# Performance work log

Hardware: AMD Instinct MI355X
Metric: run time of the kernel (lower is better)

Reference implementation:

```python
import jax, jax.numpy as jnp
import numpy as np

N = 500_000
D = 256
G = 1024


def setup_inputs() -> dict:
    key = jax.random.key(0)
    k1, k2, k3, k4, k5, k6 = jax.random.split(key, 6)
    x = jax.random.normal(k1, (N, D), dtype=jnp.float32)
    batch = jnp.sort(jax.random.randint(k2, (N,), 0, G).astype(jnp.int64))
    s = 1.0 / np.sqrt(D)
    W1 = jax.random.normal(k3, (D, D), dtype=jnp.float32) * s
    b1 = jax.random.normal(k4, (D,), dtype=jnp.float32) * 0.01
    W2 = jax.random.normal(k5, (D, 1), dtype=jnp.float32) * s
    b2 = jax.random.normal(k6, (1,), dtype=jnp.float32) * 0.01
    return {"x": x, "batch": batch, "num_graphs": G,
            "W1": W1, "b1": b1, "W2": W2, "b2": b2}


def reference(x, batch, num_graphs, W1, b1, W2, b2):
    # gate MLP: Linear -> Tanh -> Linear  => [N, 1]
    h = jnp.tanh(x @ W1 + b1)
    scores = (h @ W2 + b2)[:, 0]  # [N]
    # segment softmax over nodes grouped by graph id
    seg_max = jax.ops.segment_max(scores, batch, num_segments=num_graphs)  # [G]
    # empty segments give -inf max, but no node indexes them
    e = jnp.exp(scores - seg_max[batch])  # [N]
    denom = jax.ops.segment_sum(e, batch, num_segments=num_graphs)  # [G]
    attn = e / denom[batch]  # [N]
    weighted = x * attn[:, None]  # [N, D]
    # global_add_pool: scatter-add nodes into graphs
    return jax.ops.segment_sum(weighted, batch, num_segments=num_graphs)  # [G, D]
```

## Files before the change

### kernel.cpp

```cpp
#include <hip/hip_runtime.h>

#define D 256
#define ROWS 32
#define NBLK 512

typedef __attribute__((ext_vector_type(8))) short bf16x8;
typedef __attribute__((ext_vector_type(4))) float f32x4;

__device__ __forceinline__ unsigned short f2bf(float a) {
    unsigned int u = __float_as_uint(a);
    u = (u + 0x7fffu + ((u >> 16) & 1u)) >> 16;
    return (unsigned short)u;
}

__device__ __forceinline__ unsigned int cvt_pk_bf16(float a, float b) {
    unsigned int r;
    asm("v_cvt_pk_bf16_f32 %0, %1, %2" : "=v"(r) : "v"(a), "v"(b));
    return r;
}

__device__ __forceinline__ float fast_tanh(float v) {
    float a = __builtin_fabsf(v);
    float e = __builtin_amdgcn_exp2f(a * -2.88539008177793f);
    float t = (1.0f - e) * __builtin_amdgcn_rcpf(1.0f + e);
    return __builtin_copysignf(t, v);
}

__device__ __forceinline__ int xf_off(int c, int r, int q) {
    return ((c << 10) + (r << 5) + (q << 4)) ^ ((c & 3) << 5) ^ ((r & 4) << 2);
}

__device__ __forceinline__ void gload_lds16(const void* g, void* l) {
    __builtin_amdgcn_global_load_lds(
        (const __attribute__((address_space(1))) unsigned int*)g,
        (__attribute__((address_space(3))) unsigned int*)l, 16, 0, 0);
}

__global__ void pack_w1_k(const float* __restrict__ W1, unsigned short* __restrict__ W1p) {
    int p = blockIdx.x * 256 + threadIdx.x;
    int e  = p & 7;
    int l  = (p >> 3) & 63;
    int cb = (p >> 9) & 15;
    int kk = p >> 13;
    int k   = 32 * kk + 8 * (l >> 4) + e;
    int col = 16 * cb + (l & 15);
    W1p[p] = f2bf(W1[k * D + col]);
}

__global__ void zero_k(float* __restrict__ p, int n) {
    int i = blockIdx.x * 256 + threadIdx.x;
    if (i < n) p[i] = 0.f;
}

#define STAGE(XN, tn) do {                                                      \
    const int _r0s = (tn) * ROWS;                                               \
    _Pragma("unroll")                                                           \
    for (int _it = 0; _it < 8; ++_it) {                                         \
        const int _c = _it * 4 + w;                                             \
        const int _r = (l >> 1) ^ (_c & 3);                                     \
        const int _q = (l & 1) ^ ((_r >> 2) & 1);                               \
        int _row = _r0s + _r; _row = (_row < N) ? _row : (N - 1);               \
        gload_lds16((const char*)x + ((size_t)_row << 10) + (size_t)(((_c << 1) + _q) << 4), \
                    (char*)(XN) + (_it << 12) + (w << 10) + (l << 4));          \
    }                                                                           \
} while (0)

#define FLUSHX() do {                                                           \
    *reinterpret_cast<float4*>(&red[w][l * 4]) = a4;                            \
    int _m8 = 0x7fffffff;                                                       \
    _Pragma("unroll")                                                           \
    for (int _it = 0; _it < 8; ++_it)                                           \
        if (bg[_it] > g_cur && bg[_it] < _m8) _m8 = bg[_it];                    \
    _m8 = min(_m8, __shfl_xor(_m8, 1));  _m8 = min(_m8, __shfl_xor(_m8, 2));    \
    _m8 = min(_m8, __shfl_xor(_m8, 4));  _m8 = min(_m8, __shfl_xor(_m8, 8));    \
    _m8 = min(_m8, __shfl_xor(_m8, 16)); _m8 = min(_m8, __shfl_xor(_m8, 32));   \
    float _dw = den_p;                                                          \
    _dw += __shfl_xor(_dw, 1);  _dw += __shfl_xor(_dw, 2);                      \
    _dw += __shfl_xor(_dw, 4);  _dw += __shfl_xor(_dw, 8);                      \
    _dw += __shfl_xor(_dw, 16); _dw += __shfl_xor(_dw, 32);                     \
    if (l == 0) { gmin4[w] = _m8; denw[w] = _dw; }                              \
    asm volatile("s_waitcnt lgkmcnt(0)" ::: "memory");                          \
    __builtin_amdgcn_sched_barrier(0);                                          \
    __builtin_amdgcn_s_barrier();                                               \
    __builtin_amdgcn_sched_barrier(0);                                          \
    { const float _fs = red[0][tid] + red[1][tid] + red[2][tid] + red[3][tid];  \
      atomicAdd(&accb[(size_t)g_cur * D + tid], _fs); }                         \
    if (tid == 0)                                                               \
        atomicAdd(&den[g_cur], (denw[0] + denw[1] + denw[2] + denw[3]) * 0.015625f); \
    gnv = min(min(gmin4[0], gmin4[1]), min(gmin4[2], gmin4[3]));                \
    a4 = make_float4(0.f, 0.f, 0.f, 0.f); den_p = 0.f;                          \
    __builtin_amdgcn_s_barrier();                                               \
    __builtin_amdgcn_sched_barrier(0);                                          \
} while (0)

#define POOL(XC) do {                                                           \
    if (g_cur < 0) g_cur = g0u;                                                 \
    while (true) {                                                              \
        _Pragma("unroll")                                                       \
        for (int _it = 0; _it < 8; ++_it) {                                     \
            const int _r = 4 * _it + w;                                         \
            const float _e = (bg[_it] == g_cur) ? erow[_r] : 0.f;               \
            const float4 _v = *reinterpret_cast<const float4*>(                 \
                (const char*)(XC) + xf_off(l >> 1, _r, l & 1));                 \
            a4.x += _e * _v.x; a4.y += _e * _v.y;                               \
            a4.z += _e * _v.z; a4.w += _e * _v.w;                               \
            den_p += _e;                                                        \
        }                                                                       \
        if (glast <= g_cur) break;                                              \
        FLUSHX();                                                               \
        g_cur = gnv;                                                            \
    }                                                                           \
} while (0)

#define BODY(XC, XN) do {                                                       \
    const int _row0 = t * ROWS;                                                 \
    _Pragma("unroll")                                                           \
    for (int _it = 0; _it < 8; ++_it) {                                         \
        int _ri = _row0 + 4 * _it + w;                                          \
        bg[_it] = batch[_ri < N ? _ri : N - 1];                                 \
    }                                                                           \
    const int g0u = batch[_row0];                                               \
    int _gli = _row0 + 31;                                                      \
    const int glast = batch[_gli < N ? _gli : N - 1];                           \
    __builtin_amdgcn_sched_barrier(0);                                          \
    const bool _hn = (t + 1 < t1);                                              \
    if (_hn) {                                                                  \
        STAGE(XN, t + 1);                                                       \
        asm volatile("s_waitcnt vmcnt(8) lgkmcnt(0)" ::: "memory");             \
    } else {                                                                    \
        asm volatile("s_waitcnt vmcnt(0) lgkmcnt(0)" ::: "memory");             \
    }                                                                           \
    __builtin_amdgcn_sched_barrier(0);                                          \
    __builtin_amdgcn_s_barrier();                                               \
    __builtin_amdgcn_sched_barrier(0);                                          \
     \
    f32x4 acc[2][4];                                                            \
    _Pragma("unroll")                                                           \
    for (int _m = 0; _m < 2; ++_m)                                              \
        _Pragma("unroll")                                                       \
        for (int _n = 0; _n < 4; ++_n) acc[_m][_n] = (f32x4){0.f, 0.f, 0.f, 0.f}; \
    _Pragma("unroll")                                                           \
    for (int _kk = 0; _kk < 8; ++_kk) {                                         \
        bf16x8 _afr[2];                                                         \
        _Pragma("unroll")                                                       \
        for (int _m = 0; _m < 2; ++_m) {                                        \
            const int _rr = 16 * _m + l15;                                      \
            const int _cc = 4 * _kk + g4;                                       \
            const int _o0 = xf_off(_cc, _rr, 0);                                \
            const float4 _f0 = *reinterpret_cast<const float4*>((const char*)(XC) + _o0); \
            const float4 _f1 = *reinterpret_cast<const float4*>((const char*)(XC) + (_o0 ^ 16)); \
            uint4 _u;                                                           \
            _u.x = cvt_pk_bf16(_f0.x, _f0.y); _u.y = cvt_pk_bf16(_f0.z, _f0.w); \
            _u.z = cvt_pk_bf16(_f1.x, _f1.y); _u.w = cvt_pk_bf16(_f1.z, _f1.w); \
            _afr[_m] = *reinterpret_cast<bf16x8*>(&_u);                         \
        }                                                                       \
        _Pragma("unroll")                                                       \
        for (int _m = 0; _m < 2; ++_m)                                          \
            _Pragma("unroll")                                                   \
            for (int _n = 0; _n < 4; ++_n)                                      \
                acc[_m][_n] = __builtin_amdgcn_mfma_f32_16x16x32_bf16(          \
                    _afr[_m], bfr[_kk * 4 + _n], acc[_m][_n], 0, 0, 0);         \
    }                                                                           \
    {                                                                           \
        float _part[2][4];                                                      \
        _Pragma("unroll")                                                       \
        for (int _m = 0; _m < 2; ++_m)                                          \
            _Pragma("unroll")                                                   \
            for (int _r = 0; _r < 4; ++_r) _part[_m][_r] = 0.f;                 \
        _Pragma("unroll")                                                       \
        for (int _n = 0; _n < 4; ++_n)                                          \
            _Pragma("unroll")                                                   \
            for (int _m = 0; _m < 2; ++_m)                                      \
                _Pragma("unroll")                                               \
                for (int _r = 0; _r < 4; ++_r) {                                \
                    float _h = fast_tanh(acc[_m][_n][_r] + b1v[_n]);            \
                    _part[_m][_r] += _h * w2v[_n];                              \
                }                                                               \
        _Pragma("unroll")                                                       \
        for (int _m = 0; _m < 2; ++_m)                                          \
            _Pragma("unroll")                                                   \
            for (int _r = 0; _r < 4; ++_r) {                                    \
                float _p = _part[_m][_r];                                       \
                _p += __shfl_xor(_p, 8, 16); _p += __shfl_xor(_p, 4, 16);       \
                _p += __shfl_xor(_p, 2, 16); _p += __shfl_xor(_p, 1, 16);       \
                if (l15 == 0) scpart[w][16 * _m + 4 * g4 + _r] = _p;            \
            }                                                                   \
    }                                                                           \
    asm volatile("s_waitcnt lgkmcnt(0)" ::: "memory");                          \
    __builtin_amdgcn_sched_barrier(0);                                          \
    __builtin_amdgcn_s_barrier();                                               \
    __builtin_amdgcn_sched_barrier(0);                                          \
    if (tid < 32) {                                                             \
        float _s = scpart[0][tid] + scpart[1][tid] + scpart[2][tid] + scpart[3][tid] + b2v; \
        erow[tid] = ((_row0 + tid) < N)                                         \
                  ? __builtin_amdgcn_exp2f(_s * 1.4426950408889634f) : 0.f;     \
    }                                                                           \
    asm volatile("s_waitcnt lgkmcnt(0)" ::: "memory");                          \
    __builtin_amdgcn_sched_barrier(0);                                          \
    __builtin_amdgcn_s_barrier();                                               \
    __builtin_amdgcn_sched_barrier(0);                                          \
    POOL(XC);                                                                   \
    asm volatile("s_waitcnt lgkmcnt(0)" ::: "memory");                          \
    __builtin_amdgcn_sched_barrier(0);                                          \
    __builtin_amdgcn_s_barrier();                                               \
    __builtin_amdgcn_sched_barrier(0);                                          \
    ++t;                                                                        \
} while (0)

__global__ void __launch_bounds__(256, 2)
fused_k(const float* __restrict__ x,
        const unsigned short* __restrict__ W1p,
        const float* __restrict__ b1,
        const float* __restrict__ W2,
        const float* __restrict__ b2,
        const int* __restrict__ batch,
        int N, int NT,
        float* __restrict__ accb, float* __restrict__ den) {
    __shared__ __align__(16) char Xf0[32768];
    __shared__ __align__(16) char Xf1[32768];
    __shared__ __align__(16) float red[4][256];
    __shared__ float scpart[4][32];
    __shared__ float erow[32];
    __shared__ int   gmin4[4];
    __shared__ float denw[4];

    const int tid = threadIdx.x;
    const int w   = tid >> 6;
    const int l   = tid & 63;
    const int l15 = l & 15;
    const int g4  = l >> 4;

    const int tpb = (NT + NBLK - 1) / NBLK;
    int t = blockIdx.x * tpb;
    const int t1 = min(NT, t + tpb);
    if (t >= t1) return;

    bf16x8 bfr[32];
    #pragma unroll
    for (int kk = 0; kk < 8; ++kk)
        #pragma unroll
        for (int n = 0; n < 4; ++n)
            bfr[kk * 4 + n] = *reinterpret_cast<const bf16x8*>(
                W1p + (size_t)(((kk * 16) + (w * 4 + n)) * 64 + l) * 8);

    float b1v[4], w2v[4];
    #pragma unroll
    for (int n = 0; n < 4; ++n) {
        int col = 64 * w + 16 * n + l15;
        b1v[n] = b1[col];
        w2v[n] = W2[col];
    }
    const float b2v = b2[0];

    STAGE(Xf0, t);

    float4 a4 = make_float4(0.f, 0.f, 0.f, 0.f);
    float den_p = 0.f;
    int g_cur = -1;
    int gnv = 0;
    int bg[8];

    while (true) {
        BODY(Xf0, Xf1);
        if (t >= t1) break;
        BODY(Xf1, Xf0);
        if (t >= t1) break;
    }

    FLUSHX();
}

__global__ void __launch_bounds__(256)
norm_k(const float* __restrict__ accb, const float* __restrict__ den,
       float* __restrict__ out) {
    int g = blockIdx.x;
    float dv = den[g];
    float inv = (dv > 0.f) ? 1.0f / dv : 0.f;
    out[(size_t)g * D + threadIdx.x] = accb[(size_t)g * D + threadIdx.x] * inv;
}

extern "C" void kernel_launch(void* const* d_in, const int* in_sizes, int n_in,
                              void* d_out, int out_size, void* d_ws, size_t ws_size,
                              hipStream_t stream) {
    const float* x     = (const float*)d_in[0];
    const int*   batch = (const int*)d_in[1];
    const float* W1    = (const float*)d_in[3];
    const float* b1    = (const float*)d_in[4];
    const float* W2    = (const float*)d_in[5];
    const float* b2    = (const float*)d_in[6];
    float* out = (float*)d_out;

    const int N = in_sizes[0] / D;
    const int G = out_size / D;
    const int NT = (N + ROWS - 1) / ROWS;

    char* ws = (char*)d_ws;
    unsigned short* W1p = (unsigned short*)ws;
    float* accb = (float*)(ws + 131072);
    float* den  = (float*)(ws + 131072 + (size_t)G * D * 4);

    zero_k<<<dim3((G * D + G + 255) / 256), dim3(256), 0, stream>>>(accb, G * D + G);
    pack_w1_k<<<dim3(256), dim3(256), 0, stream>>>(W1, W1p);
    fused_k<<<dim3(min(NBLK, NT)), dim3(256), 0, stream>>>(x, W1p, b1, W2, b2, batch,
                                                           N, NT, accb, den);
    norm_k<<<dim3(G), dim3(256), 0, stream>>>(accb, den, out);
}
```

Baseline: 189.2 us.

## Stage x through registers as bf16 LDS tiles, stream W1 from global, raise occupancy

```diff
diff --git a/kernel.cpp b/kernel.cpp
--- a/kernel.cpp
+++ b/kernel.cpp
@@ -2,7 +2,7 @@
 
 #define D 256
 #define ROWS 32
-#define NBLK 512
+#define NBLK 768
 
 typedef __attribute__((ext_vector_type(8))) short bf16x8;
 typedef __attribute__((ext_vector_type(4))) float f32x4;
@@ -26,14 +26,8 @@
     return __builtin_copysignf(t, v);
 }
 
-__device__ __forceinline__ int xf_off(int c, int r, int q) {
-    return ((c << 10) + (r << 5) + (q << 4)) ^ ((c & 3) << 5) ^ ((r & 4) << 2);
-}
-
-__device__ __forceinline__ void gload_lds16(const void* g, void* l) {
-    __builtin_amdgcn_global_load_lds(
-        (const __attribute__((address_space(1))) unsigned int*)g,
-        (__attribute__((address_space(3))) unsigned int*)l, 16, 0, 0);
+__device__ __forceinline__ int xb_off(int r, int kc) {
+    return (r << 9) + ((kc << 4) ^ ((r & 7) << 4));
 }
 
 __global__ void pack_w1_k(const float* __restrict__ W1, unsigned short* __restrict__ W1p) {
@@ -52,16 +46,24 @@
     if (i < n) p[i] = 0.f;
 }
 
-#define STAGE(XN, tn) do {                                                      \
+#define STAGELOAD(XV, tn) do {                                                  \
     const int _r0s = (tn) * ROWS;                                               \
     _Pragma("unroll")                                                           \
     for (int _it = 0; _it < 8; ++_it) {                                         \
-        const int _c = _it * 4 + w;                                             \
-        const int _r = (l >> 1) ^ (_c & 3);                                     \
-        const int _q = (l & 1) ^ ((_r >> 2) & 1);                               \
-        int _row = _r0s + _r; _row = (_row < N) ? _row : (N - 1);               \
-        gload_lds16((const char*)x + ((size_t)_row << 10) + (size_t)(((_c << 1) + _q) << 4), \
-                    (char*)(XN) + (_it << 12) + (w << 10) + (l << 4));          \
+        int _row = _r0s + 4 * _it + w;                                          \
+        _row = (_row < N) ? _row : (N - 1);                                     \
+        XV[_it] = x4[(size_t)_row * 64 + l];                                    \
+    }                                                                           \
+} while (0)
+
+#define WRITELDS(LN, XV) do {                                                   \
+    _Pragma("unroll")                                                           \
+    for (int _it = 0; _it < 8; ++_it) {                                         \
+        const int _r = 4 * _it + w;                                             \
+        uint2 _u = make_uint2(cvt_pk_bf16(XV[_it].x, XV[_it].y),                \
+                              cvt_pk_bf16(XV[_it].z, XV[_it].w));               \
+        *reinterpret_cast<uint2*>((char*)(LN) +                                 \
+            ((_r << 9) + ((l << 3) ^ ((_r & 7) << 4)))) = _u;                   \
     }                                                                           \
 } while (0)
 
@@ -79,31 +81,24 @@
     _dw += __shfl_xor(_dw, 4);  _dw += __shfl_xor(_dw, 8);                      \
     _dw += __shfl_xor(_dw, 16); _dw += __shfl_xor(_dw, 32);                     \
     if (l == 0) { gmin4[w] = _m8; denw[w] = _dw; }                              \
-    asm volatile("s_waitcnt lgkmcnt(0)" ::: "memory");                          \
-    __builtin_amdgcn_sched_barrier(0);                                          \
-    __builtin_amdgcn_s_barrier();                                               \
-    __builtin_amdgcn_sched_barrier(0);                                          \
+    __syncthreads();                                                            \
     { const float _fs = red[0][tid] + red[1][tid] + red[2][tid] + red[3][tid];  \
       atomicAdd(&accb[(size_t)g_cur * D + tid], _fs); }                         \
     if (tid == 0)                                                               \
         atomicAdd(&den[g_cur], (denw[0] + denw[1] + denw[2] + denw[3]) * 0.015625f); \
     gnv = min(min(gmin4[0], gmin4[1]), min(gmin4[2], gmin4[3]));                \
     a4 = make_float4(0.f, 0.f, 0.f, 0.f); den_p = 0.f;                          \
-    __builtin_amdgcn_s_barrier();                                               \
-    __builtin_amdgcn_sched_barrier(0);                                          \
-} while (0)
-
-#define POOL(XC) do {                                                           \
+    __syncthreads();                                                            \
+} while (0)
+
+#define POOL(XV) do {                                                           \
     if (g_cur < 0) g_cur = g0u;                                                 \
     while (true) {                                                              \
         _Pragma("unroll")                                                       \
         for (int _it = 0; _it < 8; ++_it) {                                     \
-            const int _r = 4 * _it + w;                                         \
-            const float _e = (bg[_it] == g_cur) ? erow[_r] : 0.f;               \
-            const float4 _v = *reinterpret_cast<const float4*>(                 \
-                (const char*)(XC) + xf_off(l >> 1, _r, l & 1));                 \
-            a4.x += _e * _v.x; a4.y += _e * _v.y;                               \
-            a4.z += _e * _v.z; a4.w += _e * _v.w;                               \
+            const float _e = (bg[_it] == g_cur) ? erow[4 * _it + w] : 0.f;      \
+            a4.x += _e * XV[_it].x; a4.y += _e * XV[_it].y;                     \
+            a4.z += _e * XV[_it].z; a4.w += _e * XV[_it].w;                     \
             den_p += _e;                                                        \
         }                                                                       \
         if (glast <= g_cur) break;                                              \
@@ -112,7 +107,7 @@
     }                                                                           \
 } while (0)
 
-#define BODY(XC, XN) do {                                                       \
+#define BODY(LC, LN, XVC, XVN) do {                                             \
     const int _row0 = t * ROWS;                                                 \
     _Pragma("unroll")                                                           \
     for (int _it = 0; _it < 8; ++_it) {                                         \
@@ -120,47 +115,45 @@
         bg[_it] = batch[_ri < N ? _ri : N - 1];                                 \
     }                                                                           \
     const int g0u = batch[_row0];                                               \
-    int _gli = _row0 + 31;                                                      \
+    int _gli = _row0 + ROWS - 1;                                                \
     const int glast = batch[_gli < N ? _gli : N - 1];                           \
-    __builtin_amdgcn_sched_barrier(0);                                          \
     const bool _hn = (t + 1 < t1);                                              \
-    if (_hn) {                                                                  \
-        STAGE(XN, t + 1);                                                       \
-        asm volatile("s_waitcnt vmcnt(8) lgkmcnt(0)" ::: "memory");             \
-    } else {                                                                    \
-        asm volatile("s_waitcnt vmcnt(0) lgkmcnt(0)" ::: "memory");             \
-    }                                                                           \
-    __builtin_amdgcn_sched_barrier(0);                                          \
-    __builtin_amdgcn_s_barrier();                                               \
-    __builtin_amdgcn_sched_barrier(0);                                          \
+    __syncthreads();       \
      \
     f32x4 acc[2][4];                                                            \
     _Pragma("unroll")                                                           \
     for (int _m = 0; _m < 2; ++_m)                                              \
         _Pragma("unroll")                                                       \
         for (int _n = 0; _n < 4; ++_n) acc[_m][_n] = (f32x4){0.f, 0.f, 0.f, 0.f}; \
+    bf16x8 _bc[4], _bn[4];                                                      \
+    _Pragma("unroll")                                                           \
+    for (int _n = 0; _n < 4; ++_n)                                              \
+        _bc[_n] = *reinterpret_cast<const bf16x8*>(                             \
+            W1p + (size_t)(((0 * 16) + (w * 4 + _n)) * 64 + l) * 8);            \
     _Pragma("unroll")                                                           \
     for (int _kk = 0; _kk < 8; ++_kk) {                                         \
+        if (_kk < 7) {                                                          \
+            _Pragma("unroll")                                                   \
+            for (int _n = 0; _n < 4; ++_n)                                      \
+                _bn[_n] = *reinterpret_cast<const bf16x8*>(                     \
+                    W1p + (size_t)((((_kk + 1) * 16) + (w * 4 + _n)) * 64 + l) * 8); \
+        }                                                                       \
         bf16x8 _afr[2];                                                         \
         _Pragma("unroll")                                                       \
-        for (int _m = 0; _m < 2; ++_m) {                                        \
-            const int _rr = 16 * _m + l15;                                      \
-            const int _cc = 4 * _kk + g4;                                       \
-            const int _o0 = xf_off(_cc, _rr, 0);                                \
-            const float4 _f0 = *reinterpret_cast<const float4*>((const char*)(XC) + _o0); \
-            const float4 _f1 = *reinterpret_cast<const float4*>((const char*)(XC) + (_o0 ^ 16)); \
-            uint4 _u;                                                           \
-            _u.x = cvt_pk_bf16(_f0.x, _f0.y); _u.y = cvt_pk_bf16(_f0.z, _f0.w); \
-            _u.z = cvt_pk_bf16(_f1.x, _f1.y); _u.w = cvt_pk_bf16(_f1.z, _f1.w); \
-            _afr[_m] = *reinterpret_cast<bf16x8*>(&_u);                         \
-        }                                                                       \
+        for (int _m = 0; _m < 2; ++_m)                                          \
+            _afr[_m] = *reinterpret_cast<const bf16x8*>(                        \
+                (const char*)(LC) + xb_off(16 * _m + l15, 4 * _kk + g4));       \
         _Pragma("unroll")                                                       \
         for (int _m = 0; _m < 2; ++_m)                                          \
             _Pragma("unroll")                                                   \
             for (int _n = 0; _n < 4; ++_n)                                      \
                 acc[_m][_n] = __builtin_amdgcn_mfma_f32_16x16x32_bf16(          \
-                    _afr[_m], bfr[_kk * 4 + _n], acc[_m][_n], 0, 0, 0);         \
-    }                                                                           \
+                    _afr[_m], _bc[_n], acc[_m][_n], 0, 0, 0);                   \
+        _Pragma("unroll")                                                       \
+        for (int _n = 0; _n < 4; ++_n) _bc[_n] = _bn[_n];                       \
+    }                                                                           \
+    if (_hn) STAGELOAD(XVN, t + 1);   \
+              \
     {                                                                           \
         float _part[2][4];                                                      \
         _Pragma("unroll")                                                       \
@@ -186,28 +179,19 @@
                 if (l15 == 0) scpart[w][16 * _m + 4 * g4 + _r] = _p;            \
             }                                                                   \
     }                                                                           \
-    asm volatile("s_waitcnt lgkmcnt(0)" ::: "memory");                          \
-    __builtin_amdgcn_sched_barrier(0);                                          \
-    __builtin_amdgcn_s_barrier();                                               \
-    __builtin_amdgcn_sched_barrier(0);                                          \
+    __syncthreads();                                                            \
     if (tid < 32) {                                                             \
         float _s = scpart[0][tid] + scpart[1][tid] + scpart[2][tid] + scpart[3][tid] + b2v; \
         erow[tid] = ((_row0 + tid) < N)                                         \
                   ? __builtin_amdgcn_exp2f(_s * 1.4426950408889634f) : 0.f;     \
     }                                                                           \
-    asm volatile("s_waitcnt lgkmcnt(0)" ::: "memory");                          \
-    __builtin_amdgcn_sched_barrier(0);                                          \
-    __builtin_amdgcn_s_barrier();                                               \
-    __builtin_amdgcn_sched_barrier(0);                                          \
-    POOL(XC);                                                                   \
-    asm volatile("s_waitcnt lgkmcnt(0)" ::: "memory");                          \
-    __builtin_amdgcn_sched_barrier(0);                                          \
-    __builtin_amdgcn_s_barrier();                                               \
-    __builtin_amdgcn_sched_barrier(0);                                          \
+    __syncthreads();                                                            \
+    POOL(XVC);                                                                  \
+    if (_hn) WRITELDS(LN, XVN);                                                 \
     ++t;                                                                        \
 } while (0)
 
-__global__ void __launch_bounds__(256, 2)
+__global__ void __launch_bounds__(256, 3)
 fused_k(const float* __restrict__ x,
         const unsigned short* __restrict__ W1p,
         const float* __restrict__ b1,
@@ -216,8 +200,8 @@
         const int* __restrict__ batch,
         int N, int NT,
         float* __restrict__ accb, float* __restrict__ den) {
-    __shared__ __align__(16) char Xf0[32768];
-    __shared__ __align__(16) char Xf1[32768];
+    __shared__ __align__(16) char LA[16384];
+    __shared__ __align__(16) char LB[16384];
     __shared__ __align__(16) float red[4][256];
     __shared__ float scpart[4][32];
     __shared__ float erow[32];
@@ -234,14 +218,6 @@
     int t = blockIdx.x * tpb;
     const int t1 = min(NT, t + tpb);
     if (t >= t1) return;
-
-    bf16x8 bfr[32];
-    #pragma unroll
-    for (int kk = 0; kk < 8; ++kk)
-        #pragma unroll
-        for (int n = 0; n < 4; ++n)
-            bfr[kk * 4 + n] = *reinterpret_cast<const bf16x8*>(
-                W1p + (size_t)(((kk * 16) + (w * 4 + n)) * 64 + l) * 8);
 
     float b1v[4], w2v[4];
     #pragma unroll
@@ -252,7 +228,11 @@
     }
     const float b2v = b2[0];
 
-    STAGE(Xf0, t);
+    const float4* x4 = reinterpret_cast<const float4*>(x);
+    float4 xvA[8], xvB[8];
+
+    STAGELOAD(xvA, t);
+    WRITELDS(LA, xvA);
 
     float4 a4 = make_float4(0.f, 0.f, 0.f, 0.f);
     float den_p = 0.f;
@@ -261,9 +241,9 @@
     int bg[8];
 
     while (true) {
-        BODY(Xf0, Xf1);
+        BODY(LA, LB, xvA, xvB);
         if (t >= t1) break;
-        BODY(Xf1, Xf0);
+        BODY(LB, LA, xvB, xvA);
         if (t >= t1) break;
     }
 
```

Measured after the change: 514.6 us. 2.72x slower.

## Use 1024-thread blocks splitting the MLP tile across 16 waves

Applied to the files above, without the earlier changes.

```diff
diff --git a/kernel.cpp b/kernel.cpp
--- a/kernel.cpp
+++ b/kernel.cpp
@@ -2,7 +2,7 @@
 
 #define D 256
 #define ROWS 32
-#define NBLK 512
+#define NBLK 256
 
 typedef __attribute__((ext_vector_type(8))) short bf16x8;
 typedef __attribute__((ext_vector_type(4))) float f32x4;
@@ -55,13 +55,13 @@
 #define STAGE(XN, tn) do {                                                      \
     const int _r0s = (tn) * ROWS;                                               \
     _Pragma("unroll")                                                           \
-    for (int _it = 0; _it < 8; ++_it) {                                         \
-        const int _c = _it * 4 + w;                                             \
+    for (int _it = 0; _it < 2; ++_it) {                                         \
+        const int _c = _it * 16 + w;                                            \
         const int _r = (l >> 1) ^ (_c & 3);                                     \
         const int _q = (l & 1) ^ ((_r >> 2) & 1);                               \
         int _row = _r0s + _r; _row = (_row < N) ? _row : (N - 1);               \
         gload_lds16((const char*)x + ((size_t)_row << 10) + (size_t)(((_c << 1) + _q) << 4), \
-                    (char*)(XN) + (_it << 12) + (w << 10) + (l << 4));          \
+                    (char*)(XN) + (_it << 14) + (w << 10) + (l << 4));          \
     }                                                                           \
 } while (0)
 
@@ -69,7 +69,7 @@
     *reinterpret_cast<float4*>(&red[w][l * 4]) = a4;                            \
     int _m8 = 0x7fffffff;                                                       \
     _Pragma("unroll")                                                           \
-    for (int _it = 0; _it < 8; ++_it)                                           \
+    for (int _it = 0; _it < 2; ++_it)                                           \
         if (bg[_it] > g_cur && bg[_it] < _m8) _m8 = bg[_it];                    \
     _m8 = min(_m8, __shfl_xor(_m8, 1));  _m8 = min(_m8, __shfl_xor(_m8, 2));    \
     _m8 = min(_m8, __shfl_xor(_m8, 4));  _m8 = min(_m8, __shfl_xor(_m8, 8));    \
@@ -78,16 +78,26 @@
     _dw += __shfl_xor(_dw, 1);  _dw += __shfl_xor(_dw, 2);                      \
     _dw += __shfl_xor(_dw, 4);  _dw += __shfl_xor(_dw, 8);                      \
     _dw += __shfl_xor(_dw, 16); _dw += __shfl_xor(_dw, 32);                     \
-    if (l == 0) { gmin4[w] = _m8; denw[w] = _dw; }                              \
-    asm volatile("s_waitcnt lgkmcnt(0)" ::: "memory");                          \
-    __builtin_amdgcn_sched_barrier(0);                                          \
-    __builtin_amdgcn_s_barrier();                                               \
-    __builtin_amdgcn_sched_barrier(0);                                          \
-    { const float _fs = red[0][tid] + red[1][tid] + red[2][tid] + red[3][tid];  \
-      atomicAdd(&accb[(size_t)g_cur * D + tid], _fs); }                         \
-    if (tid == 0)                                                               \
-        atomicAdd(&den[g_cur], (denw[0] + denw[1] + denw[2] + denw[3]) * 0.015625f); \
-    gnv = min(min(gmin4[0], gmin4[1]), min(gmin4[2], gmin4[3]));                \
+    if (l == 0) { gmin16[w] = _m8; denw[w] = _dw; }                             \
+    asm volatile("s_waitcnt lgkmcnt(0)" ::: "memory");                          \
+    __builtin_amdgcn_sched_barrier(0);                                          \
+    __builtin_amdgcn_s_barrier();                                               \
+    __builtin_amdgcn_sched_barrier(0);                                          \
+    if (tid < 256) {                                                            \
+        float _fs = 0.f;                                                        \
+        _Pragma("unroll")                                                       \
+        for (int _j = 0; _j < 16; ++_j) _fs += red[_j][tid];                    \
+        atomicAdd(&accb[(size_t)g_cur * D + tid], _fs);                         \
+    }                                                                           \
+    if (tid == 0) {                                                             \
+        float _ds = 0.f;                                                        \
+        _Pragma("unroll")                                                       \
+        for (int _j = 0; _j < 16; ++_j) _ds += denw[_j];                        \
+        atomicAdd(&den[g_cur], _ds * 0.015625f);                                \
+    }                                                                           \
+    gnv = 0x7fffffff;                                                           \
+    _Pragma("unroll")                                                           \
+    for (int _j = 0; _j < 16; ++_j) gnv = min(gnv, gmin16[_j]);                 \
     a4 = make_float4(0.f, 0.f, 0.f, 0.f); den_p = 0.f;                          \
     __builtin_amdgcn_s_barrier();                                               \
     __builtin_amdgcn_sched_barrier(0);                                          \
@@ -97,8 +107,8 @@
     if (g_cur < 0) g_cur = g0u;                                                 \
     while (true) {                                                              \
         _Pragma("unroll")                                                       \
-        for (int _it = 0; _it < 8; ++_it) {                                     \
-            const int _r = 4 * _it + w;                                         \
+        for (int _it = 0; _it < 2; ++_it) {                                     \
+            const int _r = w + 16 * _it;                                        \
             const float _e = (bg[_it] == g_cur) ? erow[_r] : 0.f;               \
             const float4 _v = *reinterpret_cast<const float4*>(                 \
                 (const char*)(XC) + xf_off(l >> 1, _r, l & 1));                 \
@@ -115,8 +125,8 @@
 #define BODY(XC, XN) do {                                                       \
     const int _row0 = t * ROWS;                                                 \
     _Pragma("unroll")                                                           \
-    for (int _it = 0; _it < 8; ++_it) {                                         \
-        int _ri = _row0 + 4 * _it + w;                                          \
+    for (int _it = 0; _it < 2; ++_it) {                                         \
+        int _ri = _row0 + w + 16 * _it;                                         \
         bg[_it] = batch[_ri < N ? _ri : N - 1];                                 \
     }                                                                           \
     const int g0u = batch[_row0];                                               \
@@ -126,7 +136,7 @@
     const bool _hn = (t + 1 < t1);                                              \
     if (_hn) {                                                                  \
         STAGE(XN, t + 1);                                                       \
-        asm volatile("s_waitcnt vmcnt(8) lgkmcnt(0)" ::: "memory");             \
+        asm volatile("s_waitcnt vmcnt(4) lgkmcnt(0)" ::: "memory");             \
     } else {                                                                    \
         asm volatile("s_waitcnt vmcnt(0) lgkmcnt(0)" ::: "memory");             \
     }                                                                           \
@@ -134,64 +144,39 @@
     __builtin_amdgcn_s_barrier();                                               \
     __builtin_amdgcn_sched_barrier(0);                                          \
      \
-    f32x4 acc[2][4];                                                            \
-    _Pragma("unroll")                                                           \
-    for (int _m = 0; _m < 2; ++_m)                                              \
-        _Pragma("unroll")                                                       \
-        for (int _n = 0; _n < 4; ++_n) acc[_m][_n] = (f32x4){0.f, 0.f, 0.f, 0.f}; \
+    f32x4 acc0 = (f32x4){0.f, 0.f, 0.f, 0.f};                                   \
+    f32x4 acc1 = (f32x4){0.f, 0.f, 0.f, 0.f};                                   \
     _Pragma("unroll")                                                           \
     for (int _kk = 0; _kk < 8; ++_kk) {                                         \
-        bf16x8 _afr[2];                                                         \
-        _Pragma("unroll")                                                       \
-        for (int _m = 0; _m < 2; ++_m) {                                        \
-            const int _rr = 16 * _m + l15;                                      \
-            const int _cc = 4 * _kk + g4;                                       \
-            const int _o0 = xf_off(_cc, _rr, 0);                                \
-            const float4 _f0 = *reinterpret_cast<const float4*>((const char*)(XC) + _o0); \
-            const float4 _f1 = *reinterpret_cast<const float4*>((const char*)(XC) + (_o0 ^ 16)); \
-            uint4 _u;                                                           \
-            _u.x = cvt_pk_bf16(_f0.x, _f0.y); _u.y = cvt_pk_bf16(_f0.z, _f0.w); \
-            _u.z = cvt_pk_bf16(_f1.x, _f1.y); _u.w = cvt_pk_bf16(_f1.z, _f1.w); \
-            _afr[_m] = *reinterpret_cast<bf16x8*>(&_u);                         \
-        }                                                                       \
-        _Pragma("unroll")                                                       \
-        for (int _m = 0; _m < 2; ++_m)                                          \
-            _Pragma("unroll")                                                   \
-            for (int _n = 0; _n < 4; ++_n)                                      \
-                acc[_m][_n] = __builtin_amdgcn_mfma_f32_16x16x32_bf16(          \
-                    _afr[_m], bfr[_kk * 4 + _n], acc[_m][_n], 0, 0, 0);         \
-    }                                                                           \
-    {                                                                           \
-        float _part[2][4];                                                      \
-        _Pragma("unroll")                                                       \
-        for (int _m = 0; _m < 2; ++_m)                                          \
-            _Pragma("unroll")                                                   \
-            for (int _r = 0; _r < 4; ++_r) _part[_m][_r] = 0.f;                 \
-        _Pragma("unroll")                                                       \
-        for (int _n = 0; _n < 4; ++_n)                                          \
-            _Pragma("unroll")                                                   \
-            for (int _m = 0; _m < 2; ++_m)                                      \
-                _Pragma("unroll")                                               \
-                for (int _r = 0; _r < 4; ++_r) {                                \
-                    float _h = fast_tanh(acc[_m][_n][_r] + b1v[_n]);            \
-                    _part[_m][_r] += _h * w2v[_n];                              \
-                }                                                               \
-        _Pragma("unroll")                                                       \
-        for (int _m = 0; _m < 2; ++_m)                                          \
-            _Pragma("unroll")                                                   \
-            for (int _r = 0; _r < 4; ++_r) {                                    \
-                float _p = _part[_m][_r];                                       \
-                _p += __shfl_xor(_p, 8, 16); _p += __shfl_xor(_p, 4, 16);       \
-                _p += __shfl_xor(_p, 2, 16); _p += __shfl_xor(_p, 1, 16);       \
-                if (l15 == 0) scpart[w][16 * _m + 4 * g4 + _r] = _p;            \
-            }                                                                   \
+        const int _rr = 16 * rg + l15;                                          \
+        const int _cc = 4 * _kk + g4;                                           \
+        const int _o0 = xf_off(_cc, _rr, 0);                                    \
+        const float4 _f0 = *reinterpret_cast<const float4*>((const char*)(XC) + _o0); \
+        const float4 _f1 = *reinterpret_cast<const float4*>((const char*)(XC) + (_o0 ^ 16)); \
+        uint4 _u;                                                               \
+        _u.x = cvt_pk_bf16(_f0.x, _f0.y); _u.y = cvt_pk_bf16(_f0.z, _f0.w);     \
+        _u.z = cvt_pk_bf16(_f1.x, _f1.y); _u.w = cvt_pk_bf16(_f1.z, _f1.w);     \
+        const bf16x8 _afr = *reinterpret_cast<bf16x8*>(&_u);                    \
+        acc0 = __builtin_amdgcn_mfma_f32_16x16x32_bf16(_afr, bfr[_kk * 2 + 0], acc0, 0, 0, 0); \
+        acc1 = __builtin_amdgcn_mfma_f32_16x16x32_bf16(_afr, bfr[_kk * 2 + 1], acc1, 0, 0, 0); \
+    }                                                                           \
+     \
+    _Pragma("unroll")                                                           \
+    for (int _r = 0; _r < 4; ++_r) {                                            \
+        float _p = fast_tanh(acc0[_r] + b1v0) * w2v0                            \
+                 + fast_tanh(acc1[_r] + b1v1) * w2v1;                           \
+        _p += __shfl_xor(_p, 8, 16); _p += __shfl_xor(_p, 4, 16);               \
+        _p += __shfl_xor(_p, 2, 16); _p += __shfl_xor(_p, 1, 16);               \
+        if (l15 == 0) scpart[cg][16 * rg + 4 * g4 + _r] = _p;                   \
     }                                                                           \
     asm volatile("s_waitcnt lgkmcnt(0)" ::: "memory");                          \
     __builtin_amdgcn_sched_barrier(0);                                          \
     __builtin_amdgcn_s_barrier();                                               \
     __builtin_amdgcn_sched_barrier(0);                                          \
     if (tid < 32) {                                                             \
-        float _s = scpart[0][tid] + scpart[1][tid] + scpart[2][tid] + scpart[3][tid] + b2v; \
+        float _s = 0.f;                                                         \
+        _Pragma("unroll")                                                       \
+        for (int _j = 0; _j < 8; ++_j) _s += scpart[_j][tid];                   \
         erow[tid] = ((_row0 + tid) < N)                                         \
                   ? __builtin_amdgcn_exp2f(_s * 1.4426950408889634f) : 0.f;     \
     }                                                                           \
@@ -207,7 +192,7 @@
     ++t;                                                                        \
 } while (0)
 
-__global__ void __launch_bounds__(256, 2)
+__global__ void __launch_bounds__(1024)
 fused_k(const float* __restrict__ x,
         const unsigned short* __restrict__ W1p,
         const float* __restrict__ b1,
@@ -218,39 +203,37 @@
         float* __restrict__ accb, float* __restrict__ den) {
     __shared__ __align__(16) char Xf0[32768];
     __shared__ __align__(16) char Xf1[32768];
-    __shared__ __align__(16) float red[4][256];
-    __shared__ float scpart[4][32];
+    __shared__ __align__(16) float red[16][256];
+    __shared__ float scpart[8][32];
     __shared__ float erow[32];
-    __shared__ int   gmin4[4];
-    __shared__ float denw[4];
+    __shared__ int   gmin16[16];
+    __shared__ float denw[16];
 
     const int tid = threadIdx.x;
     const int w   = tid >> 6;
     const int l   = tid & 63;
     const int l15 = l & 15;
     const int g4  = l >> 4;
+    const int rg  = w >> 3;
+    const int cg  = w & 7;
 
     const int tpb = (NT + NBLK - 1) / NBLK;
     int t = blockIdx.x * tpb;
     const int t1 = min(NT, t + tpb);
     if (t >= t1) return;
 
-    bf16x8 bfr[32];
+    bf16x8 bfr[16];
     #pragma unroll
     for (int kk = 0; kk < 8; ++kk)
         #pragma unroll
-        for (int n = 0; n < 4; ++n)
-            bfr[kk * 4 + n] = *reinterpret_cast<const bf16x8*>(
-                W1p + (size_t)(((kk * 16) + (w * 4 + n)) * 64 + l) * 8);
-
-    float b1v[4], w2v[4];
-    #pragma unroll
-    for (int n = 0; n < 4; ++n) {
-        int col = 64 * w + 16 * n + l15;
-        b1v[n] = b1[col];
-        w2v[n] = W2[col];
-    }
-    const float b2v = b2[0];
+        for (int n = 0; n < 2; ++n)
+            bfr[kk * 2 + n] = *reinterpret_cast<const bf16x8*>(
+                W1p + (size_t)(((kk * 16) + (cg * 2 + n)) * 64 + l) * 8);
+
+    const float b1v0 = b1[32 * cg + l15];
+    const float b1v1 = b1[32 * cg + 16 + l15];
+    const float w2v0 = W2[32 * cg + l15];
+    const float w2v1 = W2[32 * cg + 16 + l15];
 
     STAGE(Xf0, t);
 
@@ -258,7 +241,7 @@
     float den_p = 0.f;
     int g_cur = -1;
     int gnv = 0;
-    int bg[8];
+    int bg[2];
 
     while (true) {
         BODY(Xf0, Xf1);
@@ -289,6 +272,7 @@
     const float* W2    = (const float*)d_in[5];
     const float* b2    = (const float*)d_in[6];
     float* out = (float*)d_out;
+    (void)b2;
 
     const int N = in_sizes[0] / D;
     const int G = out_size / D;
@@ -301,7 +285,7 @@
 
     zero_k<<<dim3((G * D + G + 255) / 256), dim3(256), 0, stream>>>(accb, G * D + G);
     pack_w1_k<<<dim3(256), dim3(256), 0, stream>>>(W1, W1p);
-    fused_k<<<dim3(min(NBLK, NT)), dim3(256), 0, stream>>>(x, W1p, b1, W2, b2, batch,
-                                                           N, NT, accb, den);
+    fused_k<<<dim3(min(NBLK, NT)), dim3(1024), 0, stream>>>(x, W1p, b1, W2, b2, batch,
+                                                            N, NT, accb, den);
     norm_k<<<dim3(G), dim3(256), 0, stream>>>(accb, den, out);
 }
```

Measured after the change: 310.0 us. 1.64x slower.
